# Performance work log

Measured on AMD Instinct MI355X. Metric: run time of the kernel, lower is better.

The kernel has to match this reference:

```python
import jax, jax.numpy as jnp
import numpy as np

N, M, DIM_K, DIM_V = 8192, 8192, 256, 256

def setup_inputs() -> dict:
    key = jax.random.key(0)
    kq, kk, kv = jax.random.split(key, 3)
    Q = jax.random.normal(kq, (N, DIM_K), dtype=jnp.float32)
    K = jax.random.normal(kk, (M, DIM_K), dtype=jnp.float32)
    V = jax.random.normal(kv, (M, DIM_V), dtype=jnp.float32)
    return {"Q": Q, "K": K, "V": V}

def reference(Q, K, V):
    # scores: [N, M] = Q @ K^T / sqrt(dim_k)
    scale = 1.0 / jnp.sqrt(jnp.asarray(Q.shape[-1], dtype=Q.dtype))
    scores = jnp.einsum('nd,md->nm', Q, K) * scale
    attn = jax.nn.softmax(scores, axis=-1)  # softmax over keys
    return attn @ V  # [N, dim_v]
```

## Files before the change

kernel.cpp:

```cpp
#include <hip/hip_runtime.h>
#include <hip/hip_bf16.h>
#include <hip/hip_fp16.h>


typedef __attribute__((ext_vector_type(16))) float floatx16;
typedef __attribute__((ext_vector_type(8)))  short short8;

union S8u { short8 v; unsigned short u[8]; };

#if __has_builtin(__builtin_amdgcn_exp2f)
#define EXP2F(x) __builtin_amdgcn_exp2f(x)
#else
#define EXP2F(x) exp2f(x)
#endif

__device__ __forceinline__ unsigned short f2bf(float f) {
    unsigned int u = __builtin_bit_cast(unsigned int, f);
    unsigned int r = u + 0x7fffu + ((u >> 16) & 1u);
    return (unsigned short)(r >> 16);
}

__device__ __forceinline__ unsigned cvtpk_bf16(float lo, float hi) {
    unsigned r;
    asm("v_cvt_pk_bf16_f32 %0, %1, %2" : "=v"(r) : "v"(lo), "v"(hi));
    return r;
}

__device__ __forceinline__ void gload16(const void* g, void* l) {
    __builtin_amdgcn_global_load_lds(
        (const __attribute__((address_space(1))) unsigned int*)g,
        (__attribute__((address_space(3))) unsigned int*)l, 16, 0, 0);
}


__global__ void cvt_bf16_kernel(const float* __restrict__ in,
                                unsigned short* __restrict__ out,
                                float scale, int n8) {
    int i = blockIdx.x * blockDim.x + threadIdx.x;
    if (i >= n8) return;
    const float4* p = reinterpret_cast<const float4*>(in) + (size_t)i * 2;
    float4 a = p[0], b = p[1];
    S8u r;
    r.u[0] = f2bf(a.x * scale); r.u[1] = f2bf(a.y * scale);
    r.u[2] = f2bf(a.z * scale); r.u[3] = f2bf(a.w * scale);
    r.u[4] = f2bf(b.x * scale); r.u[5] = f2bf(b.y * scale);
    r.u[6] = f2bf(b.z * scale); r.u[7] = f2bf(b.w * scale);
    *reinterpret_cast<short8*>(out + (size_t)i * 8) = r.v;
}

__global__ void transpose_v_kernel(const float* __restrict__ V,
                                   unsigned short* __restrict__ Vt) {
    __shared__ unsigned short T[64][72];
    const int kv0 = blockIdx.x * 64;
    const int v0  = blockIdx.y * 64;
    const int tid = threadIdx.x;
#pragma unroll
    for (int it = 0; it < 4; ++it) {
        int flat = it * 256 + tid;
        int r  = flat >> 4;
        int c4 = (flat & 15) * 4;
        float4 f = *reinterpret_cast<const float4*>(
            V + (size_t)(kv0 + r) * 256 + v0 + c4);
        T[c4 + 0][r] = f2bf(f.x);
        T[c4 + 1][r] = f2bf(f.y);
        T[c4 + 2][r] = f2bf(f.z);
        T[c4 + 3][r] = f2bf(f.w);
    }
    __syncthreads();
#pragma unroll
    for (int it = 0; it < 2; ++it) {
        int flat = it * 256 + tid;
        int r  = flat >> 3;
        int c8 = (flat & 7) * 8;
        short8 v8 = *reinterpret_cast<const short8*>(&T[r][c8]);
        *reinterpret_cast<short8*>(Vt + (size_t)(v0 + r) * 8192 + kv0 + c8) = v8;
    }
}


#define MFMA_B16 __builtin_amdgcn_mfma_f32_32x32x16_bf16

__global__ __launch_bounds__(512, 2)
void attn_kernel(const float* __restrict__ Qf,
                 const unsigned short* __restrict__ Kb,
                 const unsigned short* __restrict__ VtG,
                 __half* __restrict__ Opart,
                 float* __restrict__ Ml,
                 int kv_span, int gshift) {
    __shared__ __align__(16) unsigned char lds[2][65536];

    const int tid  = threadIdx.x;
    const int lane = tid & 63;
    const int w    = tid >> 6;
    const int l31  = lane & 31;
    const int h    = lane >> 5;

    const int ngm1 = (1 << gshift) - 1;
    const int id   = blockIdx.x + 32 * blockIdx.y;
    const int g    = id & ngm1;
    const int qblk = id >> gshift;
    const int kv_begin = g * kv_span;
    const int tiles = kv_span >> 6;
    const int q0 = qblk * 256 + w * 32;

    const float qs = 0.09016844005556021f;
    short8 qf[16];
    {
        const float* qp = Qf + (size_t)(q0 + l31) * 256 + h * 8;
#pragma unroll
        for (int ds = 0; ds < 16; ++ds) {
            float4 f0 = *reinterpret_cast<const float4*>(qp + ds * 16);
            float4 f1 = *reinterpret_cast<const float4*>(qp + ds * 16 + 4);
            uint4 uu;
            uu.x = cvtpk_bf16(f0.x * qs, f0.y * qs);
            uu.y = cvtpk_bf16(f0.z * qs, f0.w * qs);
            uu.z = cvtpk_bf16(f1.x * qs, f1.y * qs);
            uu.w = cvtpk_bf16(f1.z * qs, f1.w * qs);
            qf[ds] = __builtin_bit_cast(short8, uu);
        }
    }

    floatx16 o[8];
#pragma unroll
    for (int vt = 0; vt < 8; ++vt)
#pragma unroll
        for (int r = 0; r < 16; ++r) o[vt][r] = 0.f;
    float m_run = -1e30f, l_run = 0.f;

    int offk[4], offv[4];
#pragma unroll
    for (int i = 0; i < 4; ++i) {
        int j  = w * 4 + i;
        int rk = j * 2 + (lane >> 5);
        int ck = (lane & 31) ^ (rk & 7);
        offk[i] = rk * 256 + ck * 8;
        int rv = j * 8 + (lane >> 3);
        int cv = (lane & 7) ^ (rv & 7);
        offv[i] = rv * 8192 + cv * 8;
    }

    auto STAGE = [&](int kv0, int bufsel) {
        unsigned char* kb = &lds[bufsel][0];
        unsigned char* vb = &lds[bufsel][32768];
        const unsigned short* ks = Kb + (size_t)kv0 * 256;
        const unsigned short* vs = VtG + kv0;
#pragma unroll
        for (int i = 0; i < 4; ++i) {
            int j = w * 4 + i;
            gload16(ks + offk[i], kb + j * 1024);
            gload16(vs + offv[i], vb + j * 1024);
        }
    };

    STAGE(kv_begin, 0);
    asm volatile("s_waitcnt vmcnt(0)" ::: "memory");
    __syncthreads();

    const int swz = l31 & 7;

    auto buildPA = [&](const floatx16& sv, int rbase) -> short8 {
        unsigned cpk0 = cvtpk_bf16(sv[rbase + 0], sv[rbase + 1]);
        unsigned cpk1 = cvtpk_bf16(sv[rbase + 2], sv[rbase + 3]);
        unsigned cpk2 = cvtpk_bf16(sv[rbase + 4], sv[rbase + 5]);
        unsigned cpk3 = cvtpk_bf16(sv[rbase + 6], sv[rbase + 7]);
        uint4 uu;
#if __has_builtin(__builtin_amdgcn_permlane32_swap)
        auto r02 = __builtin_amdgcn_permlane32_swap((int)cpk0, (int)cpk2, false, false);
        auto r13 = __builtin_amdgcn_permlane32_swap((int)cpk1, (int)cpk3, false, false);
        uu.x = (unsigned)r02[0]; uu.y = (unsigned)r13[0];
        uu.z = (unsigned)r02[1]; uu.w = (unsigned)r13[1];
#else
        unsigned send0 = h ? cpk0 : cpk2;
        unsigned send1 = h ? cpk1 : cpk3;
        unsigned r0 = (unsigned)__shfl_xor((int)send0, 32);
        unsigned r1 = (unsigned)__shfl_xor((int)send1, 32);
        uu.x = h ? r0 : cpk0;
        uu.y = h ? r1 : cpk1;
        uu.z = h ? cpk2 : r0;
        uu.w = h ? cpk3 : r1;
#endif
        return __builtin_bit_cast(short8, uu);
    };

    auto SM_HALF = [&](floatx16& sv) {
        float t4[4];
#pragma unroll
        for (int i = 0; i < 4; ++i)
            t4[i] = fmaxf(fmaxf(sv[i], sv[i + 4]),
                          fmaxf(sv[i + 8], sv[i + 12]));
        float mt = fmaxf(fmaxf(t4[0], t4[1]), fmaxf(t4[2], t4[3]));
        mt = fmaxf(mt, __shfl_xor(mt, 32));
        if (__any(mt > m_run + 11.5f)) {
            float mnew = fmaxf(m_run, mt);
            float al = EXP2F(m_run - mnew);
            m_run = mnew;
            l_run *= al;
#pragma unroll
            for (int reg = 0; reg < 16; ++reg) {
                int srcl = ((reg & 3) + 8 * (reg >> 2)) + 4 * h;
                float alr = __shfl(al, srcl);
#pragma unroll
                for (int vt = 0; vt < 8; ++vt) o[vt][reg] *= alr;
            }
        }
#pragma unroll
        for (int r = 0; r < 16; ++r) sv[r] = EXP2F(sv[r] - m_run);
        float u[4];
#pragma unroll
        for (int i = 0; i < 4; ++i)
            u[i] = (sv[i] + sv[i + 4]) + (sv[i + 8] + sv[i + 12]);
        float lt = (u[0] + u[1]) + (u[2] + u[3]);
        lt += __shfl_xor(lt, 32);
        l_run += lt;
    };

    for (int t = 0; t < tiles; ++t) {
        const int cur = t & 1;
        if (t + 1 < tiles) STAGE(kv_begin + (t + 1) * 64, cur ^ 1);

        const unsigned char* kl = &lds[cur][0];
        const unsigned char* vl = &lds[cur][32768];

        floatx16 s0;
#pragma unroll
        for (int r = 0; r < 16; ++r) s0[r] = 0.f;
        __builtin_amdgcn_s_setprio(1);
#pragma unroll
        for (int ds = 0; ds < 16; ++ds) {
            int c0 = (ds * 2 + h) ^ swz;
            short8 a0 = *reinterpret_cast<const short8*>(
                kl + (size_t)l31 * 512 + c0 * 16);
            s0 = MFMA_B16(a0, qf[ds], s0, 0, 0, 0);
        }
        __builtin_amdgcn_s_setprio(0);

        SM_HALF(s0);

        floatx16 s1;
#pragma unroll
        for (int r = 0; r < 16; ++r) s1[r] = 0.f;
        __builtin_amdgcn_s_setprio(1);
#pragma unroll
        for (int ds = 0; ds < 16; ++ds) {
            int c0 = (ds * 2 + h) ^ swz;
            short8 a1 = *reinterpret_cast<const short8*>(
                kl + (size_t)(l31 + 32) * 512 + c0 * 16);
            s1 = MFMA_B16(a1, qf[ds], s1, 0, 0, 0);
        }
        __builtin_amdgcn_s_setprio(0);

        __builtin_amdgcn_s_setprio(1);
#pragma unroll
        for (int kk = 0; kk < 2; ++kk) {
            short8 pa = buildPA(s0, kk * 8);
            int cv = (kk * 2 + h) ^ swz;
#pragma unroll
            for (int vt = 0; vt < 8; ++vt) {
                short8 b = *reinterpret_cast<const short8*>(
                    vl + (size_t)(vt * 32 + l31) * 128 + cv * 16);
                o[vt] = MFMA_B16(pa, b, o[vt], 0, 0, 0);
            }
        }
        __builtin_amdgcn_s_setprio(0);

        SM_HALF(s1);

        __builtin_amdgcn_s_setprio(1);
#pragma unroll
        for (int kk = 0; kk < 2; ++kk) {
            short8 pa = buildPA(s1, kk * 8);
            int cv = ((kk + 2) * 2 + h) ^ swz;
#pragma unroll
            for (int vt = 0; vt < 8; ++vt) {
                short8 b = *reinterpret_cast<const short8*>(
                    vl + (size_t)(vt * 32 + l31) * 128 + cv * 16);
                o[vt] = MFMA_B16(pa, b, o[vt], 0, 0, 0);
            }
        }
        __builtin_amdgcn_s_setprio(0);

        asm volatile("s_waitcnt vmcnt(0)" ::: "memory");
        __syncthreads();
    }

    const size_t gq = (size_t)g * 8192;
    float linv = 1.0f / l_run;
#pragma unroll
    for (int reg = 0; reg < 16; ++reg) {
        int row = (reg & 3) + 8 * (reg >> 2) + 4 * h;
        float li = __shfl(linv, row);
#pragma unroll
        for (int vt = 0; vt < 8; ++vt)
            Opart[(gq + q0 + row) * 256 + vt * 32 + l31] =
                __float2half_rn(o[vt][reg] * li);
    }
    if (h == 0) {
        size_t idx = (gq + q0 + l31) * 2;
        Ml[idx]     = m_run;
        Ml[idx + 1] = l_run;
    }
}


__global__ void merge_kernel(const __half* __restrict__ Opart,
                             const float* __restrict__ Ml,
                             float* __restrict__ out, int ngroups) {
    int row = blockIdx.x;
    int col = threadIdx.x;
    float m = -1e30f;
    for (int g = 0; g < ngroups; ++g)
        m = fmaxf(m, Ml[((size_t)g * 8192 + row) * 2]);
    float den = 0.f, acc = 0.f;
    for (int g = 0; g < ngroups; ++g) {
        float wg = EXP2F(Ml[((size_t)g * 8192 + row) * 2] - m) *
                   Ml[((size_t)g * 8192 + row) * 2 + 1];
        den += wg;
        acc += wg * __half2float(Opart[((size_t)g * 8192 + row) * 256 + col]);
    }
    out[(size_t)row * 256 + col] = acc / den;
}


extern "C" void kernel_launch(void* const* d_in, const int* in_sizes, int n_in,
                              void* d_out, int out_size, void* d_ws, size_t ws_size,
                              hipStream_t stream) {
    const float* Q = (const float*)d_in[0];
    const float* K = (const float*)d_in[1];
    const float* V = (const float*)d_in[2];
    float* out = (float*)d_out;

    unsigned short* Kb = (unsigned short*)d_ws;
    unsigned short* Vt = Kb + (size_t)8192 * 256;

    const size_t base = (size_t)8192 * 256 * 2 * 2;
    const size_t osz  = (size_t)8192 * 256 * 2;
    const size_t mlsz = (size_t)8192 * 2 * 4;

    int gshift = 3;
    for (; gshift > 0; --gshift)
        if (base + ((osz + mlsz) << gshift) <= ws_size) break;
    int ng = 1 << gshift;

    __half* Opart = (__half*)((char*)d_ws + base);
    float*  Mlp   = (float*)((char*)d_ws + base + osz * (size_t)ng);

    const int n8 = 8192 * 256 / 8;
    cvt_bf16_kernel<<<n8 / 256, 256, 0, stream>>>(K, Kb, 1.0f, n8);
    transpose_v_kernel<<<dim3(128, 4), 256, 0, stream>>>(V, Vt);
    attn_kernel<<<dim3(32, ng), 512, 0, stream>>>(Q, Kb, Vt, Opart, Mlp,
                                                  8192 / ng, gshift);
    merge_kernel<<<8192, 256, 0, stream>>>(Opart, Mlp, out, ng);
}
```

Before: 142.9 us.

## Shrink attention blocks to 4 waves and 32-key tiles

```diff
diff --git a/kernel.cpp b/kernel.cpp
--- a/kernel.cpp
+++ b/kernel.cpp
@@ -80,14 +80,14 @@
 
 #define MFMA_B16 __builtin_amdgcn_mfma_f32_32x32x16_bf16
 
-__global__ __launch_bounds__(512, 2)
+__global__ __launch_bounds__(256, 2)
 void attn_kernel(const float* __restrict__ Qf,
                  const unsigned short* __restrict__ Kb,
                  const unsigned short* __restrict__ VtG,
                  __half* __restrict__ Opart,
                  float* __restrict__ Ml,
                  int kv_span, int gshift) {
-    __shared__ __align__(16) unsigned char lds[2][65536];
+    __shared__ __align__(16) unsigned char lds[2][32768];
 
     const int tid  = threadIdx.x;
     const int lane = tid & 63;
@@ -96,12 +96,12 @@
     const int h    = lane >> 5;
 
     const int ngm1 = (1 << gshift) - 1;
-    const int id   = blockIdx.x + 32 * blockIdx.y;
+    const int id   = blockIdx.x + 64 * blockIdx.y;
     const int g    = id & ngm1;
     const int qblk = id >> gshift;
     const int kv_begin = g * kv_span;
-    const int tiles = kv_span >> 6;
-    const int q0 = qblk * 256 + w * 32;
+    const int tiles = kv_span >> 5;
+    const int q0 = qblk * 128 + w * 32;
 
     const float qs = 0.09016844005556021f;
     short8 qf[16];
@@ -130,25 +130,23 @@
     int offk[4], offv[4];
 #pragma unroll
     for (int i = 0; i < 4; ++i) {
-        int j  = w * 4 + i;
-        int rk = j * 2 + (lane >> 5);
-        int ck = (lane & 31) ^ (rk & 7);
+        int j  = i * 256 + tid;
+        int rk = j >> 5, ck = (j & 31) ^ (rk & 7);
         offk[i] = rk * 256 + ck * 8;
-        int rv = j * 8 + (lane >> 3);
-        int cv = (lane & 7) ^ (rv & 7);
+        int rv = j >> 2, cv = (j & 3) ^ ((rv >> 1) & 3);
         offv[i] = rv * 8192 + cv * 8;
     }
 
     auto STAGE = [&](int kv0, int bufsel) {
         unsigned char* kb = &lds[bufsel][0];
-        unsigned char* vb = &lds[bufsel][32768];
+        unsigned char* vb = &lds[bufsel][16384];
         const unsigned short* ks = Kb + (size_t)kv0 * 256;
         const unsigned short* vs = VtG + kv0;
 #pragma unroll
         for (int i = 0; i < 4; ++i) {
-            int j = w * 4 + i;
-            gload16(ks + offk[i], kb + j * 1024);
-            gload16(vs + offv[i], vb + j * 1024);
+            int base = (i * 256 + w * 64) * 16;
+            gload16(ks + offk[i], kb + base);
+            gload16(vs + offv[i], vb + base);
         }
     };
 
@@ -156,7 +154,8 @@
     asm volatile("s_waitcnt vmcnt(0)" ::: "memory");
     __syncthreads();
 
-    const int swz = l31 & 7;
+    const int swz  = l31 & 7;
+    const int vswz = (l31 >> 1) & 3;
 
     auto buildPA = [&](const floatx16& sv, int rbase) -> short8 {
         unsigned cpk0 = cvtpk_bf16(sv[rbase + 0], sv[rbase + 1]);
@@ -182,44 +181,12 @@
         return __builtin_bit_cast(short8, uu);
     };
 
-    auto SM_HALF = [&](floatx16& sv) {
-        float t4[4];
-#pragma unroll
-        for (int i = 0; i < 4; ++i)
-            t4[i] = fmaxf(fmaxf(sv[i], sv[i + 4]),
-                          fmaxf(sv[i + 8], sv[i + 12]));
-        float mt = fmaxf(fmaxf(t4[0], t4[1]), fmaxf(t4[2], t4[3]));
-        mt = fmaxf(mt, __shfl_xor(mt, 32));
-        if (__any(mt > m_run + 11.5f)) {
-            float mnew = fmaxf(m_run, mt);
-            float al = EXP2F(m_run - mnew);
-            m_run = mnew;
-            l_run *= al;
-#pragma unroll
-            for (int reg = 0; reg < 16; ++reg) {
-                int srcl = ((reg & 3) + 8 * (reg >> 2)) + 4 * h;
-                float alr = __shfl(al, srcl);
-#pragma unroll
-                for (int vt = 0; vt < 8; ++vt) o[vt][reg] *= alr;
-            }
-        }
-#pragma unroll
-        for (int r = 0; r < 16; ++r) sv[r] = EXP2F(sv[r] - m_run);
-        float u[4];
-#pragma unroll
-        for (int i = 0; i < 4; ++i)
-            u[i] = (sv[i] + sv[i + 4]) + (sv[i + 8] + sv[i + 12]);
-        float lt = (u[0] + u[1]) + (u[2] + u[3]);
-        lt += __shfl_xor(lt, 32);
-        l_run += lt;
-    };
-
     for (int t = 0; t < tiles; ++t) {
         const int cur = t & 1;
-        if (t + 1 < tiles) STAGE(kv_begin + (t + 1) * 64, cur ^ 1);
+        if (t + 1 < tiles) STAGE(kv_begin + (t + 1) * 32, cur ^ 1);
 
         const unsigned char* kl = &lds[cur][0];
-        const unsigned char* vl = &lds[cur][32768];
+        const unsigned char* vl = &lds[cur][16384];
 
         floatx16 s0;
 #pragma unroll
@@ -234,46 +201,47 @@
         }
         __builtin_amdgcn_s_setprio(0);
 
-        SM_HALF(s0);
-
-        floatx16 s1;
-#pragma unroll
-        for (int r = 0; r < 16; ++r) s1[r] = 0.f;
-        __builtin_amdgcn_s_setprio(1);
-#pragma unroll
-        for (int ds = 0; ds < 16; ++ds) {
-            int c0 = (ds * 2 + h) ^ swz;
-            short8 a1 = *reinterpret_cast<const short8*>(
-                kl + (size_t)(l31 + 32) * 512 + c0 * 16);
-            s1 = MFMA_B16(a1, qf[ds], s1, 0, 0, 0);
-        }
-        __builtin_amdgcn_s_setprio(0);
+        {
+            float t4[4];
+#pragma unroll
+            for (int i = 0; i < 4; ++i)
+                t4[i] = fmaxf(fmaxf(s0[i], s0[i + 4]),
+                              fmaxf(s0[i + 8], s0[i + 12]));
+            float mt = fmaxf(fmaxf(t4[0], t4[1]), fmaxf(t4[2], t4[3]));
+            mt = fmaxf(mt, __shfl_xor(mt, 32));
+            if (__any(mt > m_run + 11.5f)) {
+                float mnew = fmaxf(m_run, mt);
+                float al = EXP2F(m_run - mnew);
+                m_run = mnew;
+                l_run *= al;
+#pragma unroll
+                for (int reg = 0; reg < 16; ++reg) {
+                    int srcl = ((reg & 3) + 8 * (reg >> 2)) + 4 * h;
+                    float alr = __shfl(al, srcl);
+#pragma unroll
+                    for (int vt = 0; vt < 8; ++vt) o[vt][reg] *= alr;
+                }
+            }
+#pragma unroll
+            for (int r = 0; r < 16; ++r) s0[r] = EXP2F(s0[r] - m_run);
+            float u[4];
+#pragma unroll
+            for (int i = 0; i < 4; ++i)
+                u[i] = (s0[i] + s0[i + 4]) + (s0[i + 8] + s0[i + 12]);
+            float lt = (u[0] + u[1]) + (u[2] + u[3]);
+            lt += __shfl_xor(lt, 32);
+            l_run += lt;
+        }
 
         __builtin_amdgcn_s_setprio(1);
 #pragma unroll
         for (int kk = 0; kk < 2; ++kk) {
             short8 pa = buildPA(s0, kk * 8);
-            int cv = (kk * 2 + h) ^ swz;
+            int cvs = (kk * 2 + h) ^ vswz;
 #pragma unroll
             for (int vt = 0; vt < 8; ++vt) {
                 short8 b = *reinterpret_cast<const short8*>(
-                    vl + (size_t)(vt * 32 + l31) * 128 + cv * 16);
-                o[vt] = MFMA_B16(pa, b, o[vt], 0, 0, 0);
-            }
-        }
-        __builtin_amdgcn_s_setprio(0);
-
-        SM_HALF(s1);
-
-        __builtin_amdgcn_s_setprio(1);
-#pragma unroll
-        for (int kk = 0; kk < 2; ++kk) {
-            short8 pa = buildPA(s1, kk * 8);
-            int cv = ((kk + 2) * 2 + h) ^ swz;
-#pragma unroll
-            for (int vt = 0; vt < 8; ++vt) {
-                short8 b = *reinterpret_cast<const short8*>(
-                    vl + (size_t)(vt * 32 + l31) * 128 + cv * 16);
+                    vl + (size_t)(vt * 32 + l31) * 64 + cvs * 16);
                 o[vt] = MFMA_B16(pa, b, o[vt], 0, 0, 0);
             }
         }
@@ -347,7 +315,7 @@
     const int n8 = 8192 * 256 / 8;
     cvt_bf16_kernel<<<n8 / 256, 256, 0, stream>>>(K, Kb, 1.0f, n8);
     transpose_v_kernel<<<dim3(128, 4), 256, 0, stream>>>(V, Vt);
-    attn_kernel<<<dim3(32, ng), 512, 0, stream>>>(Q, Kb, Vt, Opart, Mlp,
+    attn_kernel<<<dim3(64, ng), 256, 0, stream>>>(Q, Kb, Vt, Opart, Mlp,
                                                   8192 / ng, gshift);
     merge_kernel<<<8192, 256, 0, stream>>>(Opart, Mlp, out, ng);
 }
```

Measured after the change: 131.9 us. 7.7% less time.
